# Kernel optimization log

Measured on AMD Instinct MI355X. Metric: run time of the kernel, lower is better.

## Reference

```python
import jax, jax.numpy as jnp
import numpy as np

N_X, N_UNITS, N_Y, N_U = 64, 256, 32, 64
BATCH = 32768


def setup_inputs() -> dict:
    key = jax.random.key(0)
    ks = jax.random.split(key, 10)
    nz = 2 * N_X + N_UNITS
    return {
        "u": jax.random.normal(ks[0], (BATCH, N_U, 1), dtype=jnp.float32),
        "x0": jax.random.normal(ks[1], (BATCH, N_X, 1), dtype=jnp.float32),
        # learned parameters (scaled down so H stays well-conditioned and tanh unsaturated)
        "B_2": 0.1 * jax.random.normal(ks[2], (N_X, N_U), dtype=jnp.float32),
        "C_2": 0.1 * jax.random.normal(ks[3], (N_Y, N_X), dtype=jnp.float32),
        "D_12": 0.1 * jax.random.normal(ks[4], (N_UNITS, N_U), dtype=jnp.float32),
        "D_21": 0.1 * jax.random.normal(ks[5], (N_Y, N_UNITS), dtype=jnp.float32),
        "b": 0.1 * jax.random.normal(ks[6], (N_X + N_UNITS + N_Y, 1), dtype=jnp.float32),
        "X": (1.0 / np.sqrt(nz)) * jax.random.normal(ks[7], (nz, nz), dtype=jnp.float32),
        "Y1": 0.1 * jax.random.normal(ks[8], (N_X, N_X), dtype=jnp.float32),
        # fixed IQC multipliers (train_qsr=False): Q nsd, R=I so Rinv=I; S stored transposed
        "S_t": 0.1 * jax.random.normal(ks[9], (N_U, N_Y), dtype=jnp.float32),
        "Q": -jnp.eye(N_Y, dtype=jnp.float32),
        "Rinv": jnp.eye(N_U, dtype=jnp.float32),
    }


def _constrained_weights(B_2, C_2, D_12, D_21, X, S_t, Q, Rinv):
    """Port of REN.updateConstrainedWeights (train_qsr=False). Returns C_1, D_11, lam."""
    n_x, n_units = B_2.shape[0], D_12.shape[0]
    n_y = C_2.shape[0]
    nz = 2 * n_x + n_units
    C2_ = S_t @ C_2                       # [n_u, n_x]
    D21_ = S_t @ D_21 - D_12.T            # [n_u, n_units]
    H = X.T @ X + 1e-3 * jnp.eye(nz, dtype=X.dtype)
    lT1 = jnp.concatenate([C2_.T, D21_.T, B_2], axis=0)          # [nz, n_u]
    H = H + lT1 @ Rinv @ lT1.T
    lT2 = jnp.concatenate([C_2.T, D_21.T, jnp.zeros((n_x, n_y), dtype=X.dtype)], axis=0)
    H = H - lT2 @ Q @ lT2.T
    H_21 = H[n_x:n_x + n_units, :n_x]
    H_22 = H[n_x:n_x + n_units, n_x:n_x + n_units]
    C_1 = -H_21                           # [n_units, n_x]
    lam = 0.5 * jnp.diag(H_22)            # Lambda diagonal, > 0 since H is PD
    # L = tril(-(H_22 - diag(H_22))) == -strictly_lower(H_22)
    D_11 = -jnp.tril(H_22, k=-1)          # strictly lower triangular [n_units, n_units]
    return C_1, D_11, lam


def _forward(u, x0, B_2, C_2, D_12, D_21, b, X, Y1, S_t, Q, Rinv):
    n_x, n_units = B_2.shape[0], D_12.shape[0]
    C_1, D_11, lam = _constrained_weights(B_2, C_2, D_12, D_21, X, S_t, Q, Rinv)
    u2 = u[:, :, 0]                       # [B, n_u]
    x2 = x0[:, :, 0]                      # [B, n_x]
    b_w = b[n_x:n_x + n_units, 0]         # [n_units]
    b_y = b[n_x + n_units:, 0]            # [n_y]
    # precompute the non-recurrent part of the pre-activation for all units
    v = x2 @ C_1.T + u2 @ D_12.T + b_w    # [B, n_units]
    # NOTE: the source uses D_11 row (i_unit - 1), not i_unit (faithful to original code).
    # For i=0 the source uses term2 = 0; D_11 is strictly lower so the full-row dot
    # against the partially-filled w (zeros beyond index i) matches D_11[i-1, :i] @ w[:i].
    Drows = jnp.concatenate([jnp.zeros((1, n_units), dtype=D_11.dtype), D_11[:-1]], axis=0)
    batch = u2.shape[0]

    def step(w, i):
        wi = jnp.tanh((v[:, i] + w @ Drows[i]) / lam[i])   # [B]
        w = w.at[:, i].set(wi)
        return w, None

    w0 = jnp.zeros((batch, n_units), dtype=v.dtype)
    w, _ = jax.lax.scan(step, w0, jnp.arange(n_units))
    y = x2 @ C_2.T + w @ D_21.T + b_y     # [B, n_y]
    return y[:, :, None]                  # [B, n_y, 1]


def reference(u, x0, B_2, C_2, D_12, D_21, b, X, Y1, S_t, Q, Rinv):
    return _forward(u, x0, B_2, C_2, D_12, D_21, b, X, Y1, S_t, Q, Rinv)
```

## Files before the change

kernel.cpp:

```cpp
#include <hip/hip_runtime.h>
#include <hip/hip_bf16.h>

typedef __attribute__((ext_vector_type(8))) short short8;
typedef __attribute__((ext_vector_type(4))) float floatx4;
typedef __attribute__((ext_vector_type(2))) float floatx2;

#define MFMA16 __builtin_amdgcn_mfma_f32_16x16x32_bf16

__device__ inline unsigned short bf16_rn(float f) {
    return (unsigned short)((__float_as_uint(f) + 0x8000u) >> 16);
}
__device__ __attribute__((always_inline)) inline short8 pack8v(float4 a, float4 b) {
    union { short8 s; unsigned int u[4]; } r;
    union { __hip_bfloat162 h; unsigned int u; } c;
    c.h = __float22bfloat162_rn(make_float2(a.x, a.y)); r.u[0] = c.u;
    c.h = __float22bfloat162_rn(make_float2(a.z, a.w)); r.u[1] = c.u;
    c.h = __float22bfloat162_rn(make_float2(b.x, b.y)); r.u[2] = c.u;
    c.h = __float22bfloat162_rn(make_float2(b.z, b.w)); r.u[3] = c.u;
    return r.s;
}

__global__ __launch_bounds__(64) void ren_prep13(
    const float* __restrict__ B2, const float* __restrict__ C2,
    const float* __restrict__ D12, const float* __restrict__ D21,
    const float* __restrict__ St, const float* __restrict__ Q,
    const float* __restrict__ Rinv,
    float* __restrict__ lT1, float* __restrict__ t1,
    float* __restrict__ lT2, float* __restrict__ t2,
    unsigned short* __restrict__ Wvb, unsigned short* __restrict__ C2b,
    unsigned short* __restrict__ D21b)
{
    const int t = threadIdx.x;
    const int blk = blockIdx.x;
    if (blk >= 384) {
        const int id = (blk - 384) * 64 + t;
        if (id < 16384) {
            Wvb[(id >> 6) * 128 + 64 + (id & 63)] = bf16_rn(D12[id]);
        } else if (id < 16384 + 2048) {
            C2b[id - 16384] = bf16_rn(C2[id - 16384]);
        } else if (id < 16384 + 2048 + 8192) {
            D21b[id - 18432] = bf16_rn(D21[id - 18432]);
        }
        return;
    }

    __shared__ float stl[64 * 33];
    __shared__ float colbuf[32];
    __shared__ float s1[64];

    const int r = blk;
    const int c = t;
#pragma unroll
    for (int j = 0; j < 32; j++) {
        const int id = j * 64 + t;
        stl[(id >> 5) * 33 + (id & 31)] = St[id];
    }
    if (t < 32)
        colbuf[t] = (r < 64) ? C2[t * 64 + r]
                  : (r < 320 ? D21[t * 256 + (r - 64)] : 0.f);
    __syncthreads();

    float v1;
    if (r < 64) {
        float s = 0.f;
#pragma unroll
        for (int p = 0; p < 32; p++) s += stl[c * 33 + p] * colbuf[p];
        v1 = s;
    } else if (r < 320) {
        float s = 0.f;
#pragma unroll
        for (int p = 0; p < 32; p++) s += stl[c * 33 + p] * colbuf[p];
        v1 = s - D12[(r - 64) * 64 + c];
    } else {
        v1 = B2[(r - 320) * 64 + c];
    }
    s1[c] = v1;
    lT1[r * 64 + c] = v1;
    if (c < 32) {
        const float v2 = (r < 320) ? colbuf[c] : 0.f;
        lT2[r * 32 + c] = v2;
    }
    __syncthreads();

    float a = 0.f;
#pragma unroll
    for (int k = 0; k < 64; k++) a += s1[k] * Rinv[k * 64 + c];
    t1[r * 64 + c] = a;

    if (c < 32) {
        float bq = 0.f;
#pragma unroll
        for (int k = 0; k < 32; k++) bq += colbuf[k] * Q[k * 32 + c];
        t2[r * 32 + c] = bq;
    }
}

__global__ __launch_bounds__(320) void ren_prep2(
    const float* __restrict__ X,
    const float* __restrict__ lT1, const float* __restrict__ t1,
    const float* __restrict__ lT2, const float* __restrict__ t2,
    unsigned short* __restrict__ Wvb, unsigned short* __restrict__ Drowsb,
    float* __restrict__ Dpair, float* __restrict__ lamg)
{
    __shared__ float xcol[384];
    const int c = threadIdx.x;
    const int i = blockIdx.x;
    for (int t = c; t < 384; t += 320) xcol[t] = X[t * 384 + 64 + i];
    __syncthreads();

    float f0 = 0.f, f1 = 0.f, f2 = 0.f, f3 = 0.f;
    float ac[8], au[8], bc8[8], bu[8];
#pragma unroll
    for (int kk = 0; kk < 8; kk++) { ac[kk] = X[kk * 384 + c]; au[kk] = xcol[kk]; }
    for (int k0 = 0; k0 < 384; k0 += 16) {
#pragma unroll
        for (int kk = 0; kk < 8; kk++) {
            bc8[kk] = X[(k0 + 8 + kk) * 384 + c]; bu[kk] = xcol[k0 + 8 + kk];
        }
        f0 += au[0] * ac[0]; f1 += au[1] * ac[1];
        f2 += au[2] * ac[2]; f3 += au[3] * ac[3];
        f0 += au[4] * ac[4]; f1 += au[5] * ac[5];
        f2 += au[6] * ac[6]; f3 += au[7] * ac[7];
        if (k0 + 16 < 384) {
#pragma unroll
            for (int kk = 0; kk < 8; kk++) {
                ac[kk] = X[(k0 + 16 + kk) * 384 + c]; au[kk] = xcol[k0 + 16 + kk];
            }
        }
        f0 += bu[0] * bc8[0]; f1 += bu[1] * bc8[1];
        f2 += bu[2] * bc8[2]; f3 += bu[3] * bc8[3];
        f0 += bu[4] * bc8[4]; f1 += bu[5] * bc8[5];
        f2 += bu[6] * bc8[6]; f3 += bu[7] * bc8[7];
    }

    const float* __restrict__ t1r = t1 + (64 + i) * 64;
    const float* __restrict__ l1r = lT1 + c * 64;
#pragma unroll
    for (int m4 = 0; m4 < 16; m4++) {
        const float4 lv = *(const float4*)(l1r + m4 * 4);
        f0 += t1r[m4 * 4 + 0] * lv.x; f1 += t1r[m4 * 4 + 1] * lv.y;
        f2 += t1r[m4 * 4 + 2] * lv.z; f3 += t1r[m4 * 4 + 3] * lv.w;
    }
    const float* __restrict__ t2r = t2 + (64 + i) * 32;
    const float* __restrict__ l2r = lT2 + c * 32;
#pragma unroll
    for (int m4 = 0; m4 < 8; m4++) {
        const float4 lv = *(const float4*)(l2r + m4 * 4);
        f0 -= t2r[m4 * 4 + 0] * lv.x; f1 -= t2r[m4 * 4 + 1] * lv.y;
        f2 -= t2r[m4 * 4 + 2] * lv.z; f3 -= t2r[m4 * 4 + 3] * lv.w;
    }
    float acc = (f0 + f1) + (f2 + f3) + (((64 + i) == c) ? 0.001f : 0.f);

    if (c < 64) {
        Wvb[i * 128 + c] = bf16_rn(-acc);
    } else {
        const int cb = c - 64;
        if (cb == i) lamg[i] = 5.7707801635558536f / acc;
        if (i < 255) {
            const float dv = (cb <= i - 1) ? -acc : 0.f;
            Drowsb[(i + 1) * 256 + cb] = bf16_rn(dv);
            const int row = i + 1;
            if ((row >> 4) == (cb >> 4)) {
                const int q = row & 15, p = cb & 15;
                Dpair[(row >> 4) * 256 + (q >> 1) * 32 + p * 2 + (q & 1)] = dv;
            }
        } else {
            Drowsb[cb] = 0;
        }
    }
}

__device__ __attribute__((always_inline)) inline void triangle16x2(
    float (&vlA)[16], float (&wlA)[16],
    float (&vlB)[16], float (&wlB)[16],
    const float* __restrict__ dblk, const float* __restrict__ lam)
{
#pragma unroll
    for (int tq = 0; tq < 8; tq++) {
        floatx2 aA, bA, aB, bB;
        aA[0] = vlA[2 * tq]; aA[1] = vlA[2 * tq + 1];
        aB[0] = vlB[2 * tq]; aB[1] = vlB[2 * tq + 1];
        bA[0] = 0.f; bA[1] = 0.f;
        bB[0] = 0.f; bB[1] = 0.f;
#pragma unroll
        for (int p4 = 0; p4 < tq; p4++) {
            const float4 d4 = *(const float4*)&dblk[tq * 32 + p4 * 4];
            floatx2 de; de[0] = d4.x; de[1] = d4.y;
            floatx2 dz; dz[0] = d4.z; dz[1] = d4.w;
            aA += de * wlA[2 * p4];  bA += dz * wlA[2 * p4 + 1];
            aB += de * wlB[2 * p4];  bB += dz * wlB[2 * p4 + 1];
        }
        aA += bA; aB += bB;
        floatx2 lm2; lm2[0] = lam[2 * tq]; lm2[1] = lam[2 * tq + 1];
        aA *= lm2; aB *= lm2;
        const float e0A = __builtin_amdgcn_exp2f(aA[0]);
        const float e1A = __builtin_amdgcn_exp2f(aA[1]);
        const float e0B = __builtin_amdgcn_exp2f(aB[0]);
        const float e1B = __builtin_amdgcn_exp2f(aB[1]);
        wlA[2 * tq]     = 1.f - 2.f * __builtin_amdgcn_rcpf(e0A + 1.f);
        wlA[2 * tq + 1] = 1.f - 2.f * __builtin_amdgcn_rcpf(e1A + 1.f);
        wlB[2 * tq]     = 1.f - 2.f * __builtin_amdgcn_rcpf(e0B + 1.f);
        wlB[2 * tq + 1] = 1.f - 2.f * __builtin_amdgcn_rcpf(e1B + 1.f);
    }
}

__global__ __launch_bounds__(64, 1) void ren_main(
    const float* __restrict__ u, const float* __restrict__ x0,
    const float* __restrict__ b,
    const unsigned short* __restrict__ Wvb,
    const unsigned short* __restrict__ Drowsb,
    const float* __restrict__ Dpair,
    const float* __restrict__ lamg,
    const unsigned short* __restrict__ C2b,
    const unsigned short* __restrict__ D21b,
    float* __restrict__ out)
{
    __shared__ float bufA[16][20];
    __shared__ float bufB[16][20];
    __shared__ float dblk[256];
    __shared__ float lamsh[256];
    __shared__ float bsh[256];
    __shared__ short8 wshA[8 * 64];
    __shared__ short8 wshB[8 * 64];

    const int L = threadIdx.x;
    const int col = L & 15;
    const int quad = L >> 4;
    const int row0 = blockIdx.x * 32;

#pragma unroll
    for (int j = 0; j < 4; j++) {
        lamsh[j * 64 + L] = lamg[j * 64 + L];
        bsh[j * 64 + L]   = b[64 + j * 64 + L];
    }
    const short8 zero8 = {0, 0, 0, 0, 0, 0, 0, 0};
#pragma unroll
    for (int c = 0; c < 8; c++) { wshA[c * 64 + L] = zero8; wshB[c * 64 + L] = zero8; }

    short8 zfA[4], zfB[4];
#pragma unroll
    for (int c = 0; c < 4; c++) {
        const float* base = (c < 2 ? x0 : u);
        const float* pA = base + (long)(row0 + col) * 64 + (c & 1) * 32 + quad * 8;
        const float* pB = base + (long)(row0 + 16 + col) * 64 + (c & 1) * 32 + quad * 8;
        zfA[c] = pack8v(*(const float4*)pA, *(const float4*)(pA + 4));
        zfB[c] = pack8v(*(const float4*)pB, *(const float4*)(pB + 4));
    }

    float4 dcur = *(const float4*)(Dpair + 4 * L);
    floatx4 accA0 = {0.f, 0.f, 0.f, 0.f}, accA1 = {0.f, 0.f, 0.f, 0.f};
    floatx4 accB0 = {0.f, 0.f, 0.f, 0.f}, accB1 = {0.f, 0.f, 0.f, 0.f};
    {
        short8 v0 = *(const short8*)(Wvb + col * 128 + quad * 8);
        short8 v1 = *(const short8*)(Wvb + col * 128 + 32 + quad * 8);
        short8 v2 = *(const short8*)(Wvb + col * 128 + 64 + quad * 8);
        short8 v3 = *(const short8*)(Wvb + col * 128 + 96 + quad * 8);
        accA0 = MFMA16(zfA[0], v0, accA0, 0, 0, 0);
        accB0 = MFMA16(zfB[0], v0, accB0, 0, 0, 0);
        accA1 = MFMA16(zfA[1], v1, accA1, 0, 0, 0);
        accB1 = MFMA16(zfB[1], v1, accB1, 0, 0, 0);
        accA0 = MFMA16(zfA[2], v2, accA0, 0, 0, 0);
        accB0 = MFMA16(zfB[2], v2, accB0, 0, 0, 0);
        accA1 = MFMA16(zfA[3], v3, accA1, 0, 0, 0);
        accB1 = MFMA16(zfB[3], v3, accB1, 0, 0, 0);
    }

#pragma unroll 1
    for (int n = 0; n < 15; n++) {
        const int rb = 16 * (n + 1) + col;
        float4 dnxt = *(const float4*)(Dpair + (n + 1) * 256 + 4 * L);
        short8 vf[4];
#pragma unroll
        for (int c = 0; c < 4; c++)
            vf[c] = *(const short8*)(Wvb + rb * 128 + c * 32 + quad * 8);
        short8 hf[8];
#pragma unroll
        for (int c = 0; c < 8; c++)
            hf[c] = *(const short8*)(Drowsb + rb * 256 + c * 32 + quad * 8);

        *(float4*)&dblk[4 * L] = dcur;
        const float bwv = bsh[16 * n + col];
#pragma unroll
        for (int r = 0; r < 4; r++) {
            bufA[quad * 4 + r][col] = accA0[r] + accA1[r] + bwv;
            bufB[quad * 4 + r][col] = accB0[r] + accB1[r] + bwv;
        }

        float vlA[16], wlA[16], vlB[16], wlB[16];
#pragma unroll
        for (int p4 = 0; p4 < 4; p4++) {
            const float4 ta = *(const float4*)&bufA[col][p4 * 4];
            const float4 tb = *(const float4*)&bufB[col][p4 * 4];
            vlA[p4 * 4 + 0] = ta.x; vlA[p4 * 4 + 1] = ta.y;
            vlA[p4 * 4 + 2] = ta.z; vlA[p4 * 4 + 3] = ta.w;
            vlB[p4 * 4 + 0] = tb.x; vlB[p4 * 4 + 1] = tb.y;
            vlB[p4 * 4 + 2] = tb.z; vlB[p4 * 4 + 3] = tb.w;
        }

        triangle16x2(vlA, wlA, vlB, wlB, dblk, &lamsh[16 * n]);

        {
            float4 waA, wbA, waB, wbB;
            if (quad & 1) {
                waA = make_float4(wlA[8], wlA[9], wlA[10], wlA[11]);
                wbA = make_float4(wlA[12], wlA[13], wlA[14], wlA[15]);
                waB = make_float4(wlB[8], wlB[9], wlB[10], wlB[11]);
                wbB = make_float4(wlB[12], wlB[13], wlB[14], wlB[15]);
            } else {
                waA = make_float4(wlA[0], wlA[1], wlA[2], wlA[3]);
                wbA = make_float4(wlA[4], wlA[5], wlA[6], wlA[7]);
                waB = make_float4(wlB[0], wlB[1], wlB[2], wlB[3]);
                wbB = make_float4(wlB[4], wlB[5], wlB[6], wlB[7]);
            }
            const short8 nfA = pack8v(waA, wbA);
            const short8 nfB = pack8v(waB, wbB);
            if ((quad >> 1) == (n & 1)) {
                wshA[(n >> 1) * 64 + L] = nfA;
                wshB[(n >> 1) * 64 + L] = nfB;
            }
        }

        floatx4 aA0 = {0.f, 0.f, 0.f, 0.f}, aA1 = {0.f, 0.f, 0.f, 0.f};
        floatx4 aB0 = {0.f, 0.f, 0.f, 0.f}, aB1 = {0.f, 0.f, 0.f, 0.f};
        aA0 = MFMA16(zfA[0], vf[0], aA0, 0, 0, 0);
        aB0 = MFMA16(zfB[0], vf[0], aB0, 0, 0, 0);
        aA1 = MFMA16(zfA[1], vf[1], aA1, 0, 0, 0);
        aB1 = MFMA16(zfB[1], vf[1], aB1, 0, 0, 0);
        aA0 = MFMA16(zfA[2], vf[2], aA0, 0, 0, 0);
        aB0 = MFMA16(zfB[2], vf[2], aB0, 0, 0, 0);
        aA1 = MFMA16(zfA[3], vf[3], aA1, 0, 0, 0);
        aB1 = MFMA16(zfB[3], vf[3], aB1, 0, 0, 0);
#pragma unroll
        for (int c = 0; c < 8; c++) {
            const short8 wA = wshA[c * 64 + L];
            const short8 wB = wshB[c * 64 + L];
            if (c & 1) {
                aA1 = MFMA16(wA, hf[c], aA1, 0, 0, 0);
                aB1 = MFMA16(wB, hf[c], aB1, 0, 0, 0);
            } else {
                aA0 = MFMA16(wA, hf[c], aA0, 0, 0, 0);
                aB0 = MFMA16(wB, hf[c], aB0, 0, 0, 0);
            }
        }
        accA0 = aA0; accA1 = aA1; accB0 = aB0; accB1 = aB1;
        dcur = dnxt;
    }

    {
        *(float4*)&dblk[4 * L] = dcur;
        const float bwv = bsh[240 + col];
#pragma unroll
        for (int r = 0; r < 4; r++) {
            bufA[quad * 4 + r][col] = accA0[r] + accA1[r] + bwv;
            bufB[quad * 4 + r][col] = accB0[r] + accB1[r] + bwv;
        }

        float vlA[16], wlA[16], vlB[16], wlB[16];
#pragma unroll
        for (int p4 = 0; p4 < 4; p4++) {
            const float4 ta = *(const float4*)&bufA[col][p4 * 4];
            const float4 tb = *(const float4*)&bufB[col][p4 * 4];
            vlA[p4 * 4 + 0] = ta.x; vlA[p4 * 4 + 1] = ta.y;
            vlA[p4 * 4 + 2] = ta.z; vlA[p4 * 4 + 3] = ta.w;
            vlB[p4 * 4 + 0] = tb.x; vlB[p4 * 4 + 1] = tb.y;
            vlB[p4 * 4 + 2] = tb.z; vlB[p4 * 4 + 3] = tb.w;
        }

        triangle16x2(vlA, wlA, vlB, wlB, dblk, &lamsh[240]);

        float4 waA, wbA, waB, wbB;
        if (quad & 1) {
            waA = make_float4(wlA[8], wlA[9], wlA[10], wlA[11]);
            wbA = make_float4(wlA[12], wlA[13], wlA[14], wlA[15]);
            waB = make_float4(wlB[8], wlB[9], wlB[10], wlB[11]);
            wbB = make_float4(wlB[12], wlB[13], wlB[14], wlB[15]);
        } else {
            waA = make_float4(wlA[0], wlA[1], wlA[2], wlA[3]);
            wbA = make_float4(wlA[4], wlA[5], wlA[6], wlA[7]);
            waB = make_float4(wlB[0], wlB[1], wlB[2], wlB[3]);
            wbB = make_float4(wlB[4], wlB[5], wlB[6], wlB[7]);
        }
        const short8 nfA = pack8v(waA, wbA);
        const short8 nfB = pack8v(waB, wbB);
        if (quad >= 2) {
            wshA[7 * 64 + L] = nfA;
            wshB[7 * 64 + L] = nfB;
        }
    }

    floatx4 yA0 = {0.f, 0.f, 0.f, 0.f}, yA1 = {0.f, 0.f, 0.f, 0.f};
    floatx4 yB0 = {0.f, 0.f, 0.f, 0.f}, yB1 = {0.f, 0.f, 0.f, 0.f};
    {
        const short8 yc0 = *(const short8*)(C2b + col * 64 + quad * 8);
        const short8 yc1 = *(const short8*)(C2b + col * 64 + 32 + quad * 8);
        const short8 yc2 = *(const short8*)(C2b + (16 + col) * 64 + quad * 8);
        const short8 yc3 = *(const short8*)(C2b + (16 + col) * 64 + 32 + quad * 8);
        yA0 = MFMA16(zfA[0], yc0, yA0, 0, 0, 0);
        yB0 = MFMA16(zfB[0], yc0, yB0, 0, 0, 0);
        yA1 = MFMA16(zfA[0], yc2, yA1, 0, 0, 0);
        yB1 = MFMA16(zfB[0], yc2, yB1, 0, 0, 0);
        yA0 = MFMA16(zfA[1], yc1, yA0, 0, 0, 0);
        yB0 = MFMA16(zfB[1], yc1, yB0, 0, 0, 0);
        yA1 = MFMA16(zfA[1], yc3, yA1, 0, 0, 0);
        yB1 = MFMA16(zfB[1], yc3, yB1, 0, 0, 0);
    }
#pragma unroll
    for (int c = 0; c < 8; c++) {
        const short8 wA = wshA[c * 64 + L];
        const short8 wB = wshB[c * 64 + L];
        const short8 b0 = *(const short8*)(D21b + col * 256 + c * 32 + quad * 8);
        const short8 b1 = *(const short8*)(D21b + (16 + col) * 256 + c * 32 + quad * 8);
        yA0 = MFMA16(wA, b0, yA0, 0, 0, 0);
        yB0 = MFMA16(wB, b0, yB0, 0, 0, 0);
        yA1 = MFMA16(wA, b1, yA1, 0, 0, 0);
        yB1 = MFMA16(wB, b1, yB1, 0, 0, 0);
    }
    const float by0 = b[320 + col];
    const float by1 = b[336 + col];
#pragma unroll
    for (int r = 0; r < 4; r++) {
        out[(long)(row0 + quad * 4 + r) * 32 + col]           = yA0[r] + by0;
        out[(long)(row0 + quad * 4 + r) * 32 + 16 + col]      = yA1[r] + by1;
        out[(long)(row0 + 16 + quad * 4 + r) * 32 + col]      = yB0[r] + by0;
        out[(long)(row0 + 16 + quad * 4 + r) * 32 + 16 + col] = yB1[r] + by1;
    }
}

extern "C" void kernel_launch(void* const* d_in, const int* in_sizes, int n_in,
                              void* d_out, int out_size, void* d_ws, size_t ws_size,
                              hipStream_t stream)
{
    const float* u    = (const float*)d_in[0];
    const float* x0   = (const float*)d_in[1];
    const float* B2   = (const float*)d_in[2];
    const float* C2   = (const float*)d_in[3];
    const float* D12  = (const float*)d_in[4];
    const float* D21  = (const float*)d_in[5];
    const float* b    = (const float*)d_in[6];
    const float* X    = (const float*)d_in[7];
    const float* St   = (const float*)d_in[9];
    const float* Q    = (const float*)d_in[10];
    const float* Rinv = (const float*)d_in[11];
    float* out = (float*)d_out;

    float* ws     = (float*)d_ws;
    float* lT1    = ws;
    float* t1     = lT1 + 384 * 64;
    float* lT2    = t1 + 384 * 64;
    float* t2     = lT2 + 384 * 32;
    float* lamg   = t2 + 384 * 32;
    float* Dpair  = lamg + 256;
    unsigned short* Drowsb = (unsigned short*)(Dpair + 16 * 256);
    unsigned short* Wvb    = Drowsb + 256 * 256;
    unsigned short* C2b    = Wvb + 256 * 128;
    unsigned short* D21b   = C2b + 32 * 64;

    ren_prep13<<<dim3(800), dim3(64), 0, stream>>>(B2, C2, D12, D21, St, Q, Rinv,
                                                   lT1, t1, lT2, t2, Wvb, C2b, D21b);
    ren_prep2<<<dim3(256), dim3(320), 0, stream>>>(X, lT1, t1, lT2, t2,
                                                   Wvb, Drowsb, Dpair, lamg);

    const int batch = in_sizes[0] / 64;
    ren_main<<<dim3(batch / 32), dim3(64), 0, stream>>>(u, x0, b, Wvb, Drowsb,
                                                        Dpair, lamg, C2b, D21b, out);
}
```

Measured before the change: 126.9 us.

## Add producer wave staging weights into double-buffered swizzled LDS

The main kernel now launches two waves per block. One wave acts as a producer that loads the next block's Wv, Drows and Dpair slices from global memory into double-buffered, XOR-swizzled shared memory. The other wave runs the triangle solve and the MFMAs, reading its operands from LDS. The computed w fragments are kept in registers instead of shared memory. This is meant to hide global load latency behind the serial recurrence, at the cost of a block-wide barrier every step, more LDS, and higher register pressure.

```diff
diff --git a/kernel.cpp b/kernel.cpp
--- a/kernel.cpp
+++ b/kernel.cpp
@@ -204,7 +204,7 @@
     }
 }
 
-__global__ __launch_bounds__(64, 1) void ren_main(
+__global__ __launch_bounds__(128, 2) void ren_main(
     const float* __restrict__ u, const float* __restrict__ x0,
     const float* __restrict__ b,
     const unsigned short* __restrict__ Wvb,
@@ -215,91 +215,129 @@
     const unsigned short* __restrict__ D21b,
     float* __restrict__ out)
 {
+    __shared__ unsigned short stWv[2][2048];
+    __shared__ unsigned short stDr[2][4096];
+    __shared__ float stDp[2][256];
     __shared__ float bufA[16][20];
     __shared__ float bufB[16][20];
-    __shared__ float dblk[256];
     __shared__ float lamsh[256];
     __shared__ float bsh[256];
-    __shared__ short8 wshA[8 * 64];
-    __shared__ short8 wshB[8 * 64];
-
-    const int L = threadIdx.x;
-    const int col = L & 15;
-    const int quad = L >> 4;
+
+    const int t128 = threadIdx.x;
+    const int wid = t128 >> 6;
+    const int tl = t128 & 63;
+    const int col = tl & 15;
+    const int quad = tl >> 4;
     const int row0 = blockIdx.x * 32;
-
-#pragma unroll
-    for (int j = 0; j < 4; j++) {
-        lamsh[j * 64 + L] = lamg[j * 64 + L];
-        bsh[j * 64 + L]   = b[64 + j * 64 + L];
-    }
+    const int xw = (col & 7) << 4;
+
+    lamsh[t128]       = lamg[t128];
+    lamsh[128 + t128] = lamg[128 + t128];
+    bsh[t128]         = b[64 + t128];
+    bsh[128 + t128]   = b[64 + 128 + t128];
+
     const short8 zero8 = {0, 0, 0, 0, 0, 0, 0, 0};
-#pragma unroll
-    for (int c = 0; c < 8; c++) { wshA[c * 64 + L] = zero8; wshB[c * 64 + L] = zero8; }
-
+    short8 wfA0 = zero8, wfA1 = zero8, wfA2 = zero8, wfA3 = zero8;
+    short8 wfA4 = zero8, wfA5 = zero8, wfA6 = zero8, wfA7 = zero8;
+    short8 wfB0 = zero8, wfB1 = zero8, wfB2 = zero8, wfB3 = zero8;
+    short8 wfB4 = zero8, wfB5 = zero8, wfB6 = zero8, wfB7 = zero8;
     short8 zfA[4], zfB[4];
-#pragma unroll
-    for (int c = 0; c < 4; c++) {
-        const float* base = (c < 2 ? x0 : u);
-        const float* pA = base + (long)(row0 + col) * 64 + (c & 1) * 32 + quad * 8;
-        const float* pB = base + (long)(row0 + 16 + col) * 64 + (c & 1) * 32 + quad * 8;
-        zfA[c] = pack8v(*(const float4*)pA, *(const float4*)(pA + 4));
-        zfB[c] = pack8v(*(const float4*)pB, *(const float4*)(pB + 4));
-    }
-
-    float4 dcur = *(const float4*)(Dpair + 4 * L);
     floatx4 accA0 = {0.f, 0.f, 0.f, 0.f}, accA1 = {0.f, 0.f, 0.f, 0.f};
     floatx4 accB0 = {0.f, 0.f, 0.f, 0.f}, accB1 = {0.f, 0.f, 0.f, 0.f};
-    {
-        short8 v0 = *(const short8*)(Wvb + col * 128 + quad * 8);
-        short8 v1 = *(const short8*)(Wvb + col * 128 + 32 + quad * 8);
-        short8 v2 = *(const short8*)(Wvb + col * 128 + 64 + quad * 8);
-        short8 v3 = *(const short8*)(Wvb + col * 128 + 96 + quad * 8);
-        accA0 = MFMA16(zfA[0], v0, accA0, 0, 0, 0);
-        accB0 = MFMA16(zfB[0], v0, accB0, 0, 0, 0);
-        accA1 = MFMA16(zfA[1], v1, accA1, 0, 0, 0);
-        accB1 = MFMA16(zfB[1], v1, accB1, 0, 0, 0);
-        accA0 = MFMA16(zfA[2], v2, accA0, 0, 0, 0);
-        accB0 = MFMA16(zfB[2], v2, accB0, 0, 0, 0);
-        accA1 = MFMA16(zfA[3], v3, accA1, 0, 0, 0);
-        accB1 = MFMA16(zfB[3], v3, accB1, 0, 0, 0);
+
+    if (wid == 1) {
+        short8 w0 = *(const short8*)((const char*)Wvb + 0 * 1024 + tl * 16);
+        short8 w1 = *(const short8*)((const char*)Wvb + 1 * 1024 + tl * 16);
+        short8 w2 = *(const short8*)((const char*)Wvb + 2 * 1024 + tl * 16);
+        short8 w3 = *(const short8*)((const char*)Wvb + 3 * 1024 + tl * 16);
+        floatx4 dp = *(const floatx4*)((const char*)Dpair + tl * 16);
+#pragma unroll
+        for (int j = 0; j < 4; j++) {
+            const int o = j * 1024 + tl * 16;
+            const int row = o >> 8;
+            short8 v = (j == 0) ? w0 : (j == 1) ? w1 : (j == 2) ? w2 : w3;
+            *(short8*)((char*)&stWv[0][0] + (o ^ ((row & 7) << 4))) = v;
+        }
+        *(floatx4*)((char*)&stDp[0][0] + tl * 16) = dp;
+    } else {
+#pragma unroll
+        for (int c = 0; c < 4; c++) {
+            const float* base = (c < 2 ? x0 : u);
+            const float* pA = base + (long)(row0 + col) * 64 + (c & 1) * 32 + quad * 8;
+            const float* pB = base + (long)(row0 + 16 + col) * 64 + (c & 1) * 32 + quad * 8;
+            zfA[c] = pack8v(*(const float4*)pA, *(const float4*)(pA + 4));
+            zfB[c] = pack8v(*(const float4*)pB, *(const float4*)(pB + 4));
+        }
+    }
+    __syncthreads();
+
+    if (wid == 0) {
+        const char* wp = (const char*)&stWv[0][0];
+#pragma unroll
+        for (int c = 0; c < 4; c++) {
+            const int voff = (col << 8) + c * 64 + quad * 16;
+            const short8 v = *(const short8*)(wp + (voff ^ xw));
+            if (c & 1) { accA1 = MFMA16(zfA[c], v, accA1, 0, 0, 0);
+                         accB1 = MFMA16(zfB[c], v, accB1, 0, 0, 0); }
+            else       { accA0 = MFMA16(zfA[c], v, accA0, 0, 0, 0);
+                         accB0 = MFMA16(zfB[c], v, accB0, 0, 0, 0); }
+        }
     }
 
 #pragma unroll 1
     for (int n = 0; n < 15; n++) {
-        const int rb = 16 * (n + 1) + col;
-        float4 dnxt = *(const float4*)(Dpair + (n + 1) * 256 + 4 * L);
-        short8 vf[4];
-#pragma unroll
-        for (int c = 0; c < 4; c++)
-            vf[c] = *(const short8*)(Wvb + rb * 128 + c * 32 + quad * 8);
-        short8 hf[8];
-#pragma unroll
-        for (int c = 0; c < 8; c++)
-            hf[c] = *(const short8*)(Drowsb + rb * 256 + c * 32 + quad * 8);
-
-        *(float4*)&dblk[4 * L] = dcur;
-        const float bwv = bsh[16 * n + col];
-#pragma unroll
-        for (int r = 0; r < 4; r++) {
-            bufA[quad * 4 + r][col] = accA0[r] + accA1[r] + bwv;
-            bufB[quad * 4 + r][col] = accB0[r] + accB1[r] + bwv;
-        }
-
-        float vlA[16], wlA[16], vlB[16], wlB[16];
-#pragma unroll
-        for (int p4 = 0; p4 < 4; p4++) {
-            const float4 ta = *(const float4*)&bufA[col][p4 * 4];
-            const float4 tb = *(const float4*)&bufB[col][p4 * 4];
-            vlA[p4 * 4 + 0] = ta.x; vlA[p4 * 4 + 1] = ta.y;
-            vlA[p4 * 4 + 2] = ta.z; vlA[p4 * 4 + 3] = ta.w;
-            vlB[p4 * 4 + 0] = tb.x; vlB[p4 * 4 + 1] = tb.y;
-            vlB[p4 * 4 + 2] = tb.z; vlB[p4 * 4 + 3] = tb.w;
-        }
-
-        triangle16x2(vlA, wlA, vlB, wlB, dblk, &lamsh[16 * n]);
-
-        {
+        const int pp2 = (n + 1) & 1;
+        if (wid == 1) {
+            const char* wg = (const char*)Wvb + (long)(n + 1) * 4096 + tl * 16;
+            const char* dg = (const char*)Drowsb + (long)(n + 1) * 8192 + tl * 16;
+            short8 w0 = *(const short8*)(wg + 0 * 1024);
+            short8 w1 = *(const short8*)(wg + 1 * 1024);
+            short8 w2 = *(const short8*)(wg + 2 * 1024);
+            short8 w3 = *(const short8*)(wg + 3 * 1024);
+            short8 d0 = *(const short8*)(dg + 0 * 1024);
+            short8 d1 = *(const short8*)(dg + 1 * 1024);
+            short8 d2 = *(const short8*)(dg + 2 * 1024);
+            short8 d3 = *(const short8*)(dg + 3 * 1024);
+            short8 d4 = *(const short8*)(dg + 4 * 1024);
+            short8 d5 = *(const short8*)(dg + 5 * 1024);
+            short8 d6 = *(const short8*)(dg + 6 * 1024);
+            short8 d7 = *(const short8*)(dg + 7 * 1024);
+            floatx4 dp = *(const floatx4*)((const char*)Dpair + (long)(n + 1) * 1024 + tl * 16);
+#pragma unroll
+            for (int j = 0; j < 4; j++) {
+                const int o = j * 1024 + tl * 16;
+                const int row = o >> 8;
+                short8 v = (j == 0) ? w0 : (j == 1) ? w1 : (j == 2) ? w2 : w3;
+                *(short8*)((char*)&stWv[pp2][0] + (o ^ ((row & 7) << 4))) = v;
+            }
+#pragma unroll
+            for (int j = 0; j < 8; j++) {
+                const int o = j * 1024 + tl * 16;
+                const int row = o >> 9;
+                short8 v = (j == 0) ? d0 : (j == 1) ? d1 : (j == 2) ? d2 : (j == 3) ? d3
+                         : (j == 4) ? d4 : (j == 5) ? d5 : (j == 6) ? d6 : d7;
+                *(short8*)((char*)&stDr[pp2][0] + (o ^ ((row & 7) << 4))) = v;
+            }
+            *(floatx4*)((char*)&stDp[pp2][0] + tl * 16) = dp;
+        } else {
+            const float bwv = bsh[16 * n + col];
+#pragma unroll
+            for (int r = 0; r < 4; r++) {
+                bufA[quad * 4 + r][col] = accA0[r] + accA1[r] + bwv;
+                bufB[quad * 4 + r][col] = accB0[r] + accB1[r] + bwv;
+            }
+            float vlA[16], wlA[16], vlB[16], wlB[16];
+#pragma unroll
+            for (int p4 = 0; p4 < 4; p4++) {
+                const float4 ta = *(const float4*)&bufA[col][p4 * 4];
+                const float4 tb = *(const float4*)&bufB[col][p4 * 4];
+                vlA[p4 * 4 + 0] = ta.x; vlA[p4 * 4 + 1] = ta.y;
+                vlA[p4 * 4 + 2] = ta.z; vlA[p4 * 4 + 3] = ta.w;
+                vlB[p4 * 4 + 0] = tb.x; vlB[p4 * 4 + 1] = tb.y;
+                vlB[p4 * 4 + 2] = tb.z; vlB[p4 * 4 + 3] = tb.w;
+            }
+            triangle16x2(vlA, wlA, vlB, wlB, &stDp[n & 1][0], &lamsh[16 * n]);
+
             float4 waA, wbA, waB, wbB;
             if (quad & 1) {
                 waA = make_float4(wlA[8], wlA[9], wlA[10], wlA[11]);
@@ -314,47 +352,68 @@
             }
             const short8 nfA = pack8v(waA, wbA);
             const short8 nfB = pack8v(waB, wbB);
-            if ((quad >> 1) == (n & 1)) {
-                wshA[(n >> 1) * 64 + L] = nfA;
-                wshB[(n >> 1) * 64 + L] = nfB;
-            }
-        }
-
-        floatx4 aA0 = {0.f, 0.f, 0.f, 0.f}, aA1 = {0.f, 0.f, 0.f, 0.f};
-        floatx4 aB0 = {0.f, 0.f, 0.f, 0.f}, aB1 = {0.f, 0.f, 0.f, 0.f};
-        aA0 = MFMA16(zfA[0], vf[0], aA0, 0, 0, 0);
-        aB0 = MFMA16(zfB[0], vf[0], aB0, 0, 0, 0);
-        aA1 = MFMA16(zfA[1], vf[1], aA1, 0, 0, 0);
-        aB1 = MFMA16(zfB[1], vf[1], aB1, 0, 0, 0);
-        aA0 = MFMA16(zfA[2], vf[2], aA0, 0, 0, 0);
-        aB0 = MFMA16(zfB[2], vf[2], aB0, 0, 0, 0);
-        aA1 = MFMA16(zfA[3], vf[3], aA1, 0, 0, 0);
-        aB1 = MFMA16(zfB[3], vf[3], aB1, 0, 0, 0);
-#pragma unroll
-        for (int c = 0; c < 8; c++) {
-            const short8 wA = wshA[c * 64 + L];
-            const short8 wB = wshB[c * 64 + L];
-            if (c & 1) {
-                aA1 = MFMA16(wA, hf[c], aA1, 0, 0, 0);
-                aB1 = MFMA16(wB, hf[c], aB1, 0, 0, 0);
-            } else {
-                aA0 = MFMA16(wA, hf[c], aA0, 0, 0, 0);
-                aB0 = MFMA16(wB, hf[c], aB0, 0, 0, 0);
-            }
-        }
-        accA0 = aA0; accA1 = aA1; accB0 = aB0; accB1 = aB1;
-        dcur = dnxt;
-    }
+            const bool wr = ((quad >> 1) == (n & 1));
+            switch (n >> 1) {
+                case 0: wfA0 = wr ? nfA : wfA0; wfB0 = wr ? nfB : wfB0; break;
+                case 1: wfA1 = wr ? nfA : wfA1; wfB1 = wr ? nfB : wfB1; break;
+                case 2: wfA2 = wr ? nfA : wfA2; wfB2 = wr ? nfB : wfB2; break;
+                case 3: wfA3 = wr ? nfA : wfA3; wfB3 = wr ? nfB : wfB3; break;
+                case 4: wfA4 = wr ? nfA : wfA4; wfB4 = wr ? nfB : wfB4; break;
+                case 5: wfA5 = wr ? nfA : wfA5; wfB5 = wr ? nfB : wfB5; break;
+                case 6: wfA6 = wr ? nfA : wfA6; wfB6 = wr ? nfB : wfB6; break;
+                default: wfA7 = wr ? nfA : wfA7; wfB7 = wr ? nfB : wfB7; break;
+            }
+        }
+
+        __syncthreads();
+
+        if (wid == 0) {
+            const char* wp = (const char*)&stWv[pp2][0];
+            const char* dp = (const char*)&stDr[pp2][0];
+            floatx4 aA0 = {0.f, 0.f, 0.f, 0.f}, aA1 = {0.f, 0.f, 0.f, 0.f};
+            floatx4 aB0 = {0.f, 0.f, 0.f, 0.f}, aB1 = {0.f, 0.f, 0.f, 0.f};
+#pragma unroll
+            for (int c = 0; c < 4; c++) {
+                const int voff = (col << 8) + c * 64 + quad * 16;
+                const short8 v = *(const short8*)(wp + (voff ^ xw));
+                if (c & 1) { aA1 = MFMA16(zfA[c], v, aA1, 0, 0, 0);
+                             aB1 = MFMA16(zfB[c], v, aB1, 0, 0, 0); }
+                else       { aA0 = MFMA16(zfA[c], v, aA0, 0, 0, 0);
+                             aB0 = MFMA16(zfB[c], v, aB0, 0, 0, 0); }
+            }
+#pragma unroll
+            for (int c = 0; c < 8; c++) {
+                const int hoff = (col << 9) + c * 64 + quad * 16;
+                const short8 h = *(const short8*)(dp + (hoff ^ xw));
+                short8 wA, wB;
+                switch (c) {
+                    case 0: wA = wfA0; wB = wfB0; break;
+                    case 1: wA = wfA1; wB = wfB1; break;
+                    case 2: wA = wfA2; wB = wfB2; break;
+                    case 3: wA = wfA3; wB = wfB3; break;
+                    case 4: wA = wfA4; wB = wfB4; break;
+                    case 5: wA = wfA5; wB = wfB5; break;
+                    case 6: wA = wfA6; wB = wfB6; break;
+                    default: wA = wfA7; wB = wfB7; break;
+                }
+                if (c & 1) { aA1 = MFMA16(wA, h, aA1, 0, 0, 0);
+                             aB1 = MFMA16(wB, h, aB1, 0, 0, 0); }
+                else       { aA0 = MFMA16(wA, h, aA0, 0, 0, 0);
+                             aB0 = MFMA16(wB, h, aB0, 0, 0, 0); }
+            }
+            accA0 = aA0; accA1 = aA1; accB0 = aB0; accB1 = aB1;
+        }
+    }
+
+    if (wid != 0) return;
 
     {
-        *(float4*)&dblk[4 * L] = dcur;
         const float bwv = bsh[240 + col];
 #pragma unroll
         for (int r = 0; r < 4; r++) {
             bufA[quad * 4 + r][col] = accA0[r] + accA1[r] + bwv;
             bufB[quad * 4 + r][col] = accB0[r] + accB1[r] + bwv;
         }
-
         float vlA[16], wlA[16], vlB[16], wlB[16];
 #pragma unroll
         for (int p4 = 0; p4 < 4; p4++) {
@@ -365,8 +424,7 @@
             vlB[p4 * 4 + 0] = tb.x; vlB[p4 * 4 + 1] = tb.y;
             vlB[p4 * 4 + 2] = tb.z; vlB[p4 * 4 + 3] = tb.w;
         }
-
-        triangle16x2(vlA, wlA, vlB, wlB, dblk, &lamsh[240]);
+        triangle16x2(vlA, wlA, vlB, wlB, &stDp[1][0], &lamsh[240]);
 
         float4 waA, wbA, waB, wbB;
         if (quad & 1) {
@@ -382,10 +440,7 @@
         }
         const short8 nfA = pack8v(waA, wbA);
         const short8 nfB = pack8v(waB, wbB);
-        if (quad >= 2) {
-            wshA[7 * 64 + L] = nfA;
-            wshB[7 * 64 + L] = nfB;
-        }
+        if (quad >= 2) { wfA7 = nfA; wfB7 = nfB; }
     }
 
     floatx4 yA0 = {0.f, 0.f, 0.f, 0.f}, yA1 = {0.f, 0.f, 0.f, 0.f};
@@ -406,8 +461,17 @@
     }
 #pragma unroll
     for (int c = 0; c < 8; c++) {
-        const short8 wA = wshA[c * 64 + L];
-        const short8 wB = wshB[c * 64 + L];
+        short8 wA, wB;
+        switch (c) {
+            case 0: wA = wfA0; wB = wfB0; break;
+            case 1: wA = wfA1; wB = wfB1; break;
+            case 2: wA = wfA2; wB = wfB2; break;
+            case 3: wA = wfA3; wB = wfB3; break;
+            case 4: wA = wfA4; wB = wfB4; break;
+            case 5: wA = wfA5; wB = wfB5; break;
+            case 6: wA = wfA6; wB = wfB6; break;
+            default: wA = wfA7; wB = wfB7; break;
+        }
         const short8 b0 = *(const short8*)(D21b + col * 256 + c * 32 + quad * 8);
         const short8 b1 = *(const short8*)(D21b + (16 + col) * 256 + c * 32 + quad * 8);
         yA0 = MFMA16(wA, b0, yA0, 0, 0, 0);
@@ -461,6 +525,6 @@
                                                    Wvb, Drowsb, Dpair, lamg);
 
     const int batch = in_sizes[0] / 64;
-    ren_main<<<dim3(batch / 32), dim3(64), 0, stream>>>(u, x0, b, Wvb, Drowsb,
-                                                        Dpair, lamg, C2b, D21b, out);
-}
+    ren_main<<<dim3(batch / 32), dim3(128), 0, stream>>>(u, x0, b, Wvb, Drowsb,
+                                                         Dpair, lamg, C2b, D21b, out);
+}
```

After: 137.5 us. 1.08x slower.
